# Kernel optimization log

Measured on AMD Instinct MI355X. Metric: run time of the kernel, lower is better.

The kernel has to match this reference:

```python
import jax, jax.numpy as jnp
import numpy as np

B = 1024        # number of graphs in batch
NNODES = 64     # nodes per graph
NODE = 4        # node feature size
EDGEF = 2       # edge feature size
HID = 32        # hidden_dim
NFACT = 3       # num_factories
NE = 1024       # edges per graph (self.edges list length)


def setup_inputs() -> dict:
    key = jax.random.key(0)
    ks = jax.random.split(key, 12)
    rng = np.random.default_rng(1)
    # per-graph edge list (self.edges in the torch module)
    edges = rng.integers(0, NNODES, size=(NE, 2))
    edges_src = jnp.asarray(edges[:, 0], dtype=jnp.int32)   # [NE]
    edges_dst = jnp.asarray(edges[:, 1], dtype=jnp.int32)   # [NE]
    # batched edge_index for EdgeConv: same per-graph edges offset by b*NNODES
    offs = np.arange(B, dtype=np.int64)[:, None] * NNODES   # [B,1]
    ei_src = (edges[:, 0][None, :] + offs).reshape(-1)
    ei_dst = (edges[:, 1][None, :] + offs).reshape(-1)
    edge_index = jnp.asarray(np.stack([ei_src, ei_dst], 0), dtype=jnp.int32)  # [2, B*NE]

    N = B * NNODES
    E = B * NE
    x = jax.random.normal(ks[0], (N, NODE), dtype=jnp.float32)
    edge_attr = jax.random.normal(ks[1], (E, EDGEF), dtype=jnp.float32)
    action = jax.random.uniform(ks[2], (B, NE + NFACT), dtype=jnp.float32)

    s = 0.1
    W1 = jax.random.normal(ks[3], (2 * NODE + EDGEF, HID), dtype=jnp.float32) * s
    b1 = jnp.zeros((HID,), jnp.float32)
    W2 = jax.random.normal(ks[4], (HID, HID), dtype=jnp.float32) * s
    b2 = jnp.zeros((HID,), jnp.float32)
    D = (NODE + HID) * 2 + 1  # 73
    Wl = jax.random.normal(ks[5], (D, HID), dtype=jnp.float32) * s
    bl = jnp.zeros((HID,), jnp.float32)
    Wv = jax.random.normal(ks[6], (HID, 1), dtype=jnp.float32) * s
    bv = jnp.zeros((1,), jnp.float32)

    return {"x": x, "edge_index": edge_index, "edge_attr": edge_attr,
            "action": action, "edges_src": edges_src, "edges_dst": edges_dst,
            "W1": W1, "b1": b1, "W2": W2, "b2": b2,
            "Wl": Wl, "bl": bl, "Wv": Wv, "bv": bv}


def reference(x, edge_index, edge_attr, action, edges_src, edges_dst,
              W1, b1, W2, b2, Wl, bl, Wv, bv):
    N = x.shape[0]
    src = edge_index[0]  # flow='target_to_source': x_i = x[src], aggregate at src
    dst = edge_index[1]
    # EdgeConv message: MLP(cat[x_i, x_j, edge_attr])
    tmp = jnp.concatenate([x[src], x[dst], edge_attr], axis=1)  # [E, 10]
    msg = jax.nn.relu(tmp @ W1 + b1) @ W2 + b2                  # [E, HID]
    x_pp = jax.ops.segment_sum(msg, src, num_segments=N)        # scatter-add
    # concat node feats with conv output, split into graphs
    h = jnp.concatenate([x, x_pp], axis=1).reshape(B, NNODES, NODE + HID)  # [B,NN,36]
    # gather per-edge endpoint features
    ef = jnp.concatenate([h[:, edges_src], h[:, edges_dst]], axis=2)       # [B,NE,72]
    # factory features: last NFACT nodes duplicated
    pf = jnp.concatenate([h[:, -NFACT:], h[:, -NFACT:]], axis=-1)          # [B,NF,72]
    feats = jnp.concatenate([ef, pf], axis=1)                               # [B,NE+NF,72]
    concat = jnp.concatenate([feats, action[..., None]], axis=-1)           # [B,NE+NF,73]
    hidden = jax.nn.relu(concat @ Wl + bl)                                  # [B,NE+NF,HID]
    v = hidden @ Wv + bv                                                    # [B,NE+NF,1]
    return jnp.sum(v, axis=1).squeeze(-1)                                   # [B]
```

## Files before the change

### kernel.cpp

```cpp
#include <hip/hip_runtime.h>

#define NNODES 64
#define HID 32
#define NFACT 3
#define NE 1024
#define NROWS (NE + NFACT)
#define TPB 256
#define STR 36

#define WS_DEG  64
#define WS_TN   128
#define WS_PE   256

typedef short bf16x8 __attribute__((ext_vector_type(8)));
typedef float f32x4  __attribute__((ext_vector_type(4)));

__device__ __forceinline__ short f2bf(float f) {
    unsigned u = __builtin_bit_cast(unsigned, f);
    u += 0x7fffu + ((u >> 16) & 1u);
    return (short)(u >> 16);
}
__device__ __forceinline__ float4 fma4(float a, float4 w, float4 c) {
    c.x = fmaf(a, w.x, c.x); c.y = fmaf(a, w.y, c.y);
    c.z = fmaf(a, w.z, c.z); c.w = fmaf(a, w.w, c.w);
    return c;
}

__global__ __launch_bounds__(TPB) void build_csr(const int* __restrict__ es,
                                                 int* __restrict__ ws) {
    __shared__ int sdeg[NNODES], soff[NNODES], scnt[NNODES], snt;
    const int tid = threadIdx.x;
    if (tid < NNODES) { sdeg[tid] = 0; scnt[tid] = 0; }
    __syncthreads();
#pragma unroll 1
    for (int e = tid; e < NE; e += TPB) atomicAdd(&sdeg[es[e]], 1);
    __syncthreads();
    if (tid == 0) {
        int run = 0;
#pragma unroll 1
        for (int n = 0; n < NNODES; n++) { soff[n] = run; run += (sdeg[n] + 15) >> 4; }
        snt = run;
        ws[0] = run;
    }
    __syncthreads();
    const int ntiles = snt;
    if (tid < NNODES) {
        ws[WS_DEG + tid] = sdeg[tid];
        const int base = soff[tid], cnt = (sdeg[tid] + 15) >> 4;
#pragma unroll 1
        for (int j = 0; j < cnt; j++) ws[WS_TN + base + j] = tid;
    }
#pragma unroll 1
    for (int i = tid; i < ntiles * 16; i += TPB) ws[WS_PE + i] = -1;
    __syncthreads();
#pragma unroll 1
    for (int e = tid; e < NE; e += TPB) {
        const int n = es[e];
        const int idx = atomicAdd(&scnt[n], 1);
        ws[WS_PE + soff[n] * 16 + idx] = e;
    }
}

__global__ __launch_bounds__(TPB, 4) void critic_fused(
    const float* __restrict__ x,
    const float* __restrict__ edge_attr,
    const float* __restrict__ action,
    const int*   __restrict__ es,
    const int*   __restrict__ ed,
    const float* __restrict__ W1,
    const float* __restrict__ b1,
    const float* __restrict__ W2,
    const float* __restrict__ b2,
    const float* __restrict__ Wl,
    const float* __restrict__ bl,
    const float* __restrict__ Wv,
    const float* __restrict__ bv,
    const int*   __restrict__ csr,
    float* __restrict__ out)
{
    const int b    = blockIdx.x;
    const int tid  = threadIdx.x;
    const int lane = tid & 63;
    const int wv   = tid >> 6;

    __shared__ float4 xs4[NNODES];
    __shared__ float  xpp[NNODES * STR];
    __shared__ float  qp0[NNODES * STR];
    __shared__ float  qp1[NNODES * STR];
    __shared__ float  W1s[10 * HID];
    __shared__ float  Wls[73 * HID];
    __shared__ float  b1s[HID], bls[HID], b2s[HID];
    __shared__ float  wred[TPB / 64];

    if (tid < NNODES) xs4[tid] = ((const float4*)x)[b * NNODES + tid];
    {
        float4*       W1s4 = (float4*)W1s;
        const float4* W1g  = (const float4*)W1;
        if (tid < 80) W1s4[tid] = W1g[tid];
        float4*       Wls4 = (float4*)Wls;
        const float4* Wlg  = (const float4*)Wl;
#pragma unroll 1
        for (int i = tid; i < 73 * HID / 4; i += TPB) Wls4[i] = Wlg[i];
        if (tid < HID) { b1s[tid] = b1[tid]; bls[tid] = bl[tid]; b2s[tid] = b2[tid]; }
    }
#pragma unroll 1
    for (int i = tid; i < NNODES * STR; i += TPB) xpp[i] = 0.0f;
    __syncthreads();

    const int n  = tid & 63;
    const int k0 = (tid >> 6) * 8;

    {
        const float4 xv = xs4[n];
        const float4* b1v = (const float4*)&b1s[k0];
        float4 q1a = b1v[0], q1b = b1v[1];
        float4 q2a = make_float4(0.f, 0.f, 0.f, 0.f), q2b = q2a;
#pragma unroll 1
        for (int i = 0; i < 4; i++) {
            const float xi = (i == 0) ? xv.x : (i == 1) ? xv.y : (i == 2) ? xv.z : xv.w;
            const float4* wa = (const float4*)&W1s[i * HID + k0];
            const float4* wb = (const float4*)&W1s[(4 + i) * HID + k0];
            q1a = fma4(xi, wa[0], q1a); q1b = fma4(xi, wa[1], q1b);
            q2a = fma4(xi, wb[0], q2a); q2b = fma4(xi, wb[1], q2b);
        }
        float4* q1w = (float4*)&qp0[n * STR + k0];
        float4* q2w = (float4*)&qp1[n * STR + k0];
        q1w[0] = q1a; q1w[1] = q1b;
        q2w[0] = q2a; q2w[1] = q2b;
    }
    __syncthreads();

    {
        const float2* ea2 = (const float2*)edge_attr + (size_t)b * NE;
        const int quad = lane >> 4;
        const int m16  = lane & 15;
        const int kh   = quad * 8;

        const float4* w8p = (const float4*)&W1s[8 * HID + kh];
        const float4* w9p = (const float4*)&W1s[9 * HID + kh];
        const float4 w8a = w8p[0], w8b = w8p[1];
        const float4 w9a = w9p[0], w9b = w9p[1];

        bf16x8 bf0, bf1;
#pragma unroll
        for (int j = 0; j < 8; j++) {
            bf0[j] = f2bf(W2[(kh + j) * HID + m16]);
            bf1[j] = f2bf(W2[(kh + j) * HID + 16 + m16]);
        }

        const int  ntiles = csr[0];
        const int* tile_node = csr + WS_TN;
        const int* pe        = csr + WS_PE;

#pragma unroll 1
        for (int t = wv; t < ntiles; t += TPB / 64) {
            const int node = tile_node[t];
            const int e    = pe[t * 16 + m16];
            const int esafe = (e < 0) ? 0 : e;
            const int d0   = ed[esafe];
            const float2 ea = ea2[esafe];

            const float4* Ap = (const float4*)&qp0[node * STR + kh];
            const float4  A0 = Ap[0], A1 = Ap[1];
            const float4* Gp = (const float4*)&qp1[d0 * STR + kh];
            const float4  G0 = Gp[0], G1 = Gp[1];

            bf16x8 af;
            {
                float h;
                h = A0.x + G0.x + ea.x * w8a.x + ea.y * w9a.x; af[0] = (e < 0) ? (short)0 : f2bf(fmaxf(h, 0.f));
                h = A0.y + G0.y + ea.x * w8a.y + ea.y * w9a.y; af[1] = (e < 0) ? (short)0 : f2bf(fmaxf(h, 0.f));
                h = A0.z + G0.z + ea.x * w8a.z + ea.y * w9a.z; af[2] = (e < 0) ? (short)0 : f2bf(fmaxf(h, 0.f));
                h = A0.w + G0.w + ea.x * w8a.w + ea.y * w9a.w; af[3] = (e < 0) ? (short)0 : f2bf(fmaxf(h, 0.f));
                h = A1.x + G1.x + ea.x * w8b.x + ea.y * w9b.x; af[4] = (e < 0) ? (short)0 : f2bf(fmaxf(h, 0.f));
                h = A1.y + G1.y + ea.x * w8b.y + ea.y * w9b.y; af[5] = (e < 0) ? (short)0 : f2bf(fmaxf(h, 0.f));
                h = A1.z + G1.z + ea.x * w8b.z + ea.y * w9b.z; af[6] = (e < 0) ? (short)0 : f2bf(fmaxf(h, 0.f));
                h = A1.w + G1.w + ea.x * w8b.w + ea.y * w9b.w; af[7] = (e < 0) ? (short)0 : f2bf(fmaxf(h, 0.f));
            }

            f32x4 c0 = {0.f, 0.f, 0.f, 0.f};
            f32x4 c1 = {0.f, 0.f, 0.f, 0.f};
            c0 = __builtin_amdgcn_mfma_f32_16x16x32_bf16(af, bf0, c0, 0, 0, 0);
            c1 = __builtin_amdgcn_mfma_f32_16x16x32_bf16(af, bf1, c1, 0, 0, 0);

            float s0 = c0[0] + c0[1] + c0[2] + c0[3];
            float s1 = c1[0] + c1[1] + c1[2] + c1[3];
            s0 += __shfl_xor(s0, 16); s0 += __shfl_xor(s0, 32);
            s1 += __shfl_xor(s1, 16); s1 += __shfl_xor(s1, 32);
            if (lane < 32)
                atomicAdd(&xpp[node * STR + lane], (lane < 16) ? s0 : s1);
        }
    }
    __syncthreads();

    {
        const float4 xv = xs4[n];
        const float dn = (float)csr[WS_DEG + n];
        const float4* blv = (const float4*)&bls[k0];
        float4 p1a = blv[0], p1b = blv[1];
        float4 p2a = make_float4(0.f, 0.f, 0.f, 0.f), p2b = p2a;
#pragma unroll 1
        for (int i = 0; i < 4; i++) {
            const float xi = (i == 0) ? xv.x : (i == 1) ? xv.y : (i == 2) ? xv.z : xv.w;
            const float4* wa = (const float4*)&Wls[i * HID + k0];
            const float4* wb = (const float4*)&Wls[(36 + i) * HID + k0];
            p1a = fma4(xi, wa[0], p1a); p1b = fma4(xi, wa[1], p1b);
            p2a = fma4(xi, wb[0], p2a); p2b = fma4(xi, wb[1], p2b);
        }
        const float4* xrv  = (const float4*)&xpp[n * STR];
        const float4* b2v4 = (const float4*)b2s;
#pragma unroll 1
        for (int q = 0; q < 8; q++) {
            float4 xq = xrv[q];
            const float4 bq = b2v4[q];
            xq.x = fmaf(dn, bq.x, xq.x); xq.y = fmaf(dn, bq.y, xq.y);
            xq.z = fmaf(dn, bq.z, xq.z); xq.w = fmaf(dn, bq.w, xq.w);
            const int j = q * 4;
#pragma unroll
            for (int u = 0; u < 4; u++) {
                const float xj = (u == 0) ? xq.x : (u == 1) ? xq.y : (u == 2) ? xq.z : xq.w;
                const float4* wa = (const float4*)&Wls[(4 + j + u) * HID + k0];
                const float4* wb = (const float4*)&Wls[(40 + j + u) * HID + k0];
                p1a = fma4(xj, wa[0], p1a); p1b = fma4(xj, wa[1], p1b);
                p2a = fma4(xj, wb[0], p2a); p2b = fma4(xj, wb[1], p2b);
            }
        }
        float4* p1w = (float4*)&qp0[n * STR + k0];
        float4* p2w = (float4*)&qp1[n * STR + k0];
        p1w[0] = p1a; p1w[1] = p1b;
        p2w[0] = p2a; p2w[1] = p2b;
    }
    __syncthreads();

    float vsum = 0.0f;
    {
        const float* actb = action + (size_t)b * NROWS;
        const float bvv = bv[0];
        const float* Wl72 = Wl + 72 * HID;
#pragma unroll 1
        for (int r = tid; r < NROWS; r += TPB) {
            int na, nb;
            if (r < NE) { na = es[r]; nb = ed[r]; }
            else        { na = NNODES - NFACT + (r - NE); nb = na; }
            const float a = actb[r];
            const float4* p1v = (const float4*)&qp0[na * STR];
            const float4* p2v = (const float4*)&qp1[nb * STR];
            float v = bvv;
#pragma unroll 1
            for (int q = 0; q < 8; q += 2) {
                const float4 pa0 = p1v[q],     pb0 = p2v[q];
                const float4 pa1 = p1v[q + 1], pb1 = p2v[q + 1];
                const int k = q * 4;
                v += fmaxf(pa0.x + pb0.x + a * Wl72[k+0], 0.f) * Wv[k+0];
                v += fmaxf(pa0.y + pb0.y + a * Wl72[k+1], 0.f) * Wv[k+1];
                v += fmaxf(pa0.z + pb0.z + a * Wl72[k+2], 0.f) * Wv[k+2];
                v += fmaxf(pa0.w + pb0.w + a * Wl72[k+3], 0.f) * Wv[k+3];
                v += fmaxf(pa1.x + pb1.x + a * Wl72[k+4], 0.f) * Wv[k+4];
                v += fmaxf(pa1.y + pb1.y + a * Wl72[k+5], 0.f) * Wv[k+5];
                v += fmaxf(pa1.z + pb1.z + a * Wl72[k+6], 0.f) * Wv[k+6];
                v += fmaxf(pa1.w + pb1.w + a * Wl72[k+7], 0.f) * Wv[k+7];
            }
            vsum += v;
        }
    }

#pragma unroll
    for (int off = 32; off > 0; off >>= 1)
        vsum += __shfl_down(vsum, off, 64);
    if ((tid & 63) == 0) wred[tid >> 6] = vsum;
    __syncthreads();
    if (tid == 0) {
        float t = 0.0f;
#pragma unroll
        for (int w = 0; w < TPB / 64; w++) t += wred[w];
        out[b] = t;
    }
}

extern "C" void kernel_launch(void* const* d_in, const int* in_sizes, int n_in,
                              void* d_out, int out_size, void* d_ws, size_t ws_size,
                              hipStream_t stream) {
    const float* x         = (const float*)d_in[0];
    const float* edge_attr = (const float*)d_in[2];
    const float* action    = (const float*)d_in[3];
    const int*   es        = (const int*)d_in[4];
    const int*   ed        = (const int*)d_in[5];
    const float* W1        = (const float*)d_in[6];
    const float* b1        = (const float*)d_in[7];
    const float* W2        = (const float*)d_in[8];
    const float* b2        = (const float*)d_in[9];
    const float* Wl        = (const float*)d_in[10];
    const float* bl        = (const float*)d_in[11];
    const float* Wv        = (const float*)d_in[12];
    const float* bv        = (const float*)d_in[13];
    float* out = (float*)d_out;
    int*   ws  = (int*)d_ws;

    build_csr<<<dim3(1), dim3(TPB), 0, stream>>>(es, ws);
    critic_fused<<<dim3(out_size), dim3(TPB), 0, stream>>>(
        x, edge_attr, action, es, ed, W1, b1, W2, b2, Wl, bl, Wv, bv, ws, out);
}
```

Measured before the change: 149.8 us.

## Pack dst into CSR entries, fix tile count, and software-pipeline edge loops

The CSR build now packs the destination node into the high 16 bits of each edge entry. This removes the dependent load of ed[] in the message loop. The message loop runs a fixed tile count (NTILES=128) with a two-deep register prefetch of CSR entries, node ids and edge attributes, and packs bf16 pairs directly. The readout loop also prefetches the next row's indices and action value, and handles the factory rows separately. Padding tiles add wasted MFMA work, and correctness relies on the tile count never exceeding 128 and edge ids fitting in 16 bits.

```diff
diff --git a/kernel.cpp b/kernel.cpp
--- a/kernel.cpp
+++ b/kernel.cpp
@@ -7,6 +7,7 @@
 #define NROWS (NE + NFACT)
 #define TPB 256
 #define STR 36
+#define NTILES 128
 
 #define WS_DEG  64
 #define WS_TN   128
@@ -15,6 +16,13 @@
 typedef short bf16x8 __attribute__((ext_vector_type(8)));
 typedef float f32x4  __attribute__((ext_vector_type(4)));
 
+__device__ __forceinline__ unsigned pack_bf2(float lo, float hi) {
+    unsigned ul = __builtin_bit_cast(unsigned, lo);
+    unsigned uh = __builtin_bit_cast(unsigned, hi);
+    ul += 0x7fffu + ((ul >> 16) & 1u);
+    uh += 0x7fffu + ((uh >> 16) & 1u);
+    return (ul >> 16) | (uh & 0xffff0000u);
+}
 __device__ __forceinline__ short f2bf(float f) {
     unsigned u = __builtin_bit_cast(unsigned, f);
     u += 0x7fffu + ((u >> 16) & 1u);
@@ -27,10 +35,14 @@
 }
 
 __global__ __launch_bounds__(TPB) void build_csr(const int* __restrict__ es,
+                                                 const int* __restrict__ ed,
                                                  int* __restrict__ ws) {
-    __shared__ int sdeg[NNODES], soff[NNODES], scnt[NNODES], snt;
+    __shared__ int sdeg[NNODES], soff[NNODES], scnt[NNODES];
     const int tid = threadIdx.x;
     if (tid < NNODES) { sdeg[tid] = 0; scnt[tid] = 0; }
+    if (tid < NTILES) ws[WS_TN + tid] = 0;
+#pragma unroll 1
+    for (int i = tid; i < NTILES * 16; i += TPB) ws[WS_PE + i] = 0xFFFF;
     __syncthreads();
 #pragma unroll 1
     for (int e = tid; e < NE; e += TPB) atomicAdd(&sdeg[es[e]], 1);
@@ -39,25 +51,20 @@
         int run = 0;
 #pragma unroll 1
         for (int n = 0; n < NNODES; n++) { soff[n] = run; run += (sdeg[n] + 15) >> 4; }
-        snt = run;
-        ws[0] = run;
-    }
-    __syncthreads();
-    const int ntiles = snt;
+    }
+    __syncthreads();
     if (tid < NNODES) {
         ws[WS_DEG + tid] = sdeg[tid];
         const int base = soff[tid], cnt = (sdeg[tid] + 15) >> 4;
 #pragma unroll 1
         for (int j = 0; j < cnt; j++) ws[WS_TN + base + j] = tid;
     }
-#pragma unroll 1
-    for (int i = tid; i < ntiles * 16; i += TPB) ws[WS_PE + i] = -1;
     __syncthreads();
 #pragma unroll 1
     for (int e = tid; e < NE; e += TPB) {
         const int n = es[e];
         const int idx = atomicAdd(&scnt[n], 1);
-        ws[WS_PE + soff[n] * 16 + idx] = e;
+        ws[WS_PE + soff[n] * 16 + idx] = e | (ed[e] << 16);
     }
 }
 
@@ -135,6 +142,8 @@
         const int quad = lane >> 4;
         const int m16  = lane & 15;
         const int kh   = quad * 8;
+        const int NW   = TPB / 64;
+        const int NIT  = NTILES / (TPB / 64);
 
         const float4* w8p = (const float4*)&W1s[8 * HID + kh];
         const float4* w9p = (const float4*)&W1s[9 * HID + kh];
@@ -148,35 +157,54 @@
             bf1[j] = f2bf(W2[(kh + j) * HID + 16 + m16]);
         }
 
-        const int  ntiles = csr[0];
-        const int* tile_node = csr + WS_TN;
-        const int* pe        = csr + WS_PE;
-
-#pragma unroll 1
-        for (int t = wv; t < ntiles; t += TPB / 64) {
-            const int node = tile_node[t];
-            const int e    = pe[t * 16 + m16];
-            const int esafe = (e < 0) ? 0 : e;
-            const int d0   = ed[esafe];
-            const float2 ea = ea2[esafe];
-
+        const int* tn  = csr + WS_TN;
+        const int* pep = csr + WS_PE;
+
+        int raw0  = pep[wv * 16 + m16];
+        int node0 = tn[wv];
+        int raw1  = pep[(wv + NW) * 16 + m16];
+        int node1 = tn[wv + NW];
+        {
+            const int e0 = raw0 & 0xFFFF;
+        }
+        const int e00 = raw0 & 0xFFFF;
+        float2 ea0 = ea2[(e00 == 0xFFFF) ? 0 : e00];
+
+#pragma unroll 1
+        for (int i = 0; i < NIT; i++) {
+            const int t = wv + i * NW;
+            int raw2 = 0xFFFF, node2 = 0;
+            if (i + 2 < NIT) {
+                raw2  = pep[(t + 2 * NW) * 16 + m16];
+                node2 = tn[t + 2 * NW];
+            }
+            const int e1 = raw1 & 0xFFFF;
+            const float2 ea1 = ea2[(e1 == 0xFFFF) ? 0 : e1];
+
+            const int  node = node0;
+            const bool pad  = (raw0 & 0xFFFF) == 0xFFFF;
+            const int  d0   = raw0 >> 16;
             const float4* Ap = (const float4*)&qp0[node * STR + kh];
             const float4  A0 = Ap[0], A1 = Ap[1];
             const float4* Gp = (const float4*)&qp1[d0 * STR + kh];
             const float4  G0 = Gp[0], G1 = Gp[1];
 
-            bf16x8 af;
-            {
-                float h;
-                h = A0.x + G0.x + ea.x * w8a.x + ea.y * w9a.x; af[0] = (e < 0) ? (short)0 : f2bf(fmaxf(h, 0.f));
-                h = A0.y + G0.y + ea.x * w8a.y + ea.y * w9a.y; af[1] = (e < 0) ? (short)0 : f2bf(fmaxf(h, 0.f));
-                h = A0.z + G0.z + ea.x * w8a.z + ea.y * w9a.z; af[2] = (e < 0) ? (short)0 : f2bf(fmaxf(h, 0.f));
-                h = A0.w + G0.w + ea.x * w8a.w + ea.y * w9a.w; af[3] = (e < 0) ? (short)0 : f2bf(fmaxf(h, 0.f));
-                h = A1.x + G1.x + ea.x * w8b.x + ea.y * w9b.x; af[4] = (e < 0) ? (short)0 : f2bf(fmaxf(h, 0.f));
-                h = A1.y + G1.y + ea.x * w8b.y + ea.y * w9b.y; af[5] = (e < 0) ? (short)0 : f2bf(fmaxf(h, 0.f));
-                h = A1.z + G1.z + ea.x * w8b.z + ea.y * w9b.z; af[6] = (e < 0) ? (short)0 : f2bf(fmaxf(h, 0.f));
-                h = A1.w + G1.w + ea.x * w8b.w + ea.y * w9b.w; af[7] = (e < 0) ? (short)0 : f2bf(fmaxf(h, 0.f));
-            }
+            float h0, h1, h2, h3, h4, h5, h6, h7;
+            h0 = fmaxf(A0.x + G0.x + ea0.x * w8a.x + ea0.y * w9a.x, 0.f);
+            h1 = fmaxf(A0.y + G0.y + ea0.x * w8a.y + ea0.y * w9a.y, 0.f);
+            h2 = fmaxf(A0.z + G0.z + ea0.x * w8a.z + ea0.y * w9a.z, 0.f);
+            h3 = fmaxf(A0.w + G0.w + ea0.x * w8a.w + ea0.y * w9a.w, 0.f);
+            h4 = fmaxf(A1.x + G1.x + ea0.x * w8b.x + ea0.y * w9b.x, 0.f);
+            h5 = fmaxf(A1.y + G1.y + ea0.x * w8b.y + ea0.y * w9b.y, 0.f);
+            h6 = fmaxf(A1.z + G1.z + ea0.x * w8b.z + ea0.y * w9b.z, 0.f);
+            h7 = fmaxf(A1.w + G1.w + ea0.x * w8b.w + ea0.y * w9b.w, 0.f);
+
+            uint4 packed;
+            packed.x = pad ? 0u : pack_bf2(h0, h1);
+            packed.y = pad ? 0u : pack_bf2(h2, h3);
+            packed.z = pad ? 0u : pack_bf2(h4, h5);
+            packed.w = pad ? 0u : pack_bf2(h6, h7);
+            const bf16x8 af = __builtin_bit_cast(bf16x8, packed);
 
             f32x4 c0 = {0.f, 0.f, 0.f, 0.f};
             f32x4 c1 = {0.f, 0.f, 0.f, 0.f};
@@ -189,6 +217,9 @@
             s1 += __shfl_xor(s1, 16); s1 += __shfl_xor(s1, 32);
             if (lane < 32)
                 atomicAdd(&xpp[node * STR + lane], (lane < 16) ? s0 : s1);
+
+            raw0 = raw1; node0 = node1; ea0 = ea1;
+            raw1 = raw2; node1 = node2;
         }
     }
     __syncthreads();
@@ -237,14 +268,42 @@
         const float* actb = action + (size_t)b * NROWS;
         const float bvv = bv[0];
         const float* Wl72 = Wl + 72 * HID;
-#pragma unroll 1
-        for (int r = tid; r < NROWS; r += TPB) {
-            int na, nb;
-            if (r < NE) { na = es[r]; nb = ed[r]; }
-            else        { na = NNODES - NFACT + (r - NE); nb = na; }
+
+        int na0 = es[tid], nb0 = ed[tid];
+        float a0 = actb[tid];
+#pragma unroll 1
+        for (int i = 0; i < 4; i++) {
+            int na1 = 0, nb1 = 0; float a1 = 0.f;
+            if (i < 3) {
+                const int rn = tid + (i + 1) * TPB;
+                na1 = es[rn]; nb1 = ed[rn]; a1 = actb[rn];
+            }
+            const float4* p1v = (const float4*)&qp0[na0 * STR];
+            const float4* p2v = (const float4*)&qp1[nb0 * STR];
+            float v = bvv;
+#pragma unroll 1
+            for (int q = 0; q < 8; q += 2) {
+                const float4 pa0 = p1v[q],     pb0 = p2v[q];
+                const float4 pa1 = p1v[q + 1], pb1 = p2v[q + 1];
+                const int k = q * 4;
+                v += fmaxf(pa0.x + pb0.x + a0 * Wl72[k+0], 0.f) * Wv[k+0];
+                v += fmaxf(pa0.y + pb0.y + a0 * Wl72[k+1], 0.f) * Wv[k+1];
+                v += fmaxf(pa0.z + pb0.z + a0 * Wl72[k+2], 0.f) * Wv[k+2];
+                v += fmaxf(pa0.w + pb0.w + a0 * Wl72[k+3], 0.f) * Wv[k+3];
+                v += fmaxf(pa1.x + pb1.x + a0 * Wl72[k+4], 0.f) * Wv[k+4];
+                v += fmaxf(pa1.y + pb1.y + a0 * Wl72[k+5], 0.f) * Wv[k+5];
+                v += fmaxf(pa1.z + pb1.z + a0 * Wl72[k+6], 0.f) * Wv[k+6];
+                v += fmaxf(pa1.w + pb1.w + a0 * Wl72[k+7], 0.f) * Wv[k+7];
+            }
+            vsum += v;
+            na0 = na1; nb0 = nb1; a0 = a1;
+        }
+        if (tid < NFACT) {
+            const int r = NE + tid;
+            const int na = NNODES - NFACT + tid;
             const float a = actb[r];
             const float4* p1v = (const float4*)&qp0[na * STR];
-            const float4* p2v = (const float4*)&qp1[nb * STR];
+            const float4* p2v = (const float4*)&qp1[na * STR];
             float v = bvv;
 #pragma unroll 1
             for (int q = 0; q < 8; q += 2) {
@@ -296,7 +355,7 @@
     float* out = (float*)d_out;
     int*   ws  = (int*)d_ws;
 
-    build_csr<<<dim3(1), dim3(TPB), 0, stream>>>(es, ws);
+    build_csr<<<dim3(1), dim3(TPB), 0, stream>>>(es, ed, ws);
     critic_fused<<<dim3(out_size), dim3(TPB), 0, stream>>>(
         x, edge_attr, action, es, ed, W1, b1, W2, b2, Wl, bl, Wv, bv, ws, out);
 }
```

Measured after the change: 149.4 us. About the same (-0.2%).
